# Kernel tuning notes

Hardware: AMD Instinct MI355X
Metric: run time of the kernel (lower is better)

## Reference

```python
import jax, jax.numpy as jnp
import numpy as np
from jax import lax

LAMBDA_REG = 0.01


def setup_inputs() -> dict:
    key = jax.random.key(0)
    k1, k2 = jax.random.split(key)
    features = jax.random.normal(k1, (8192, 512), dtype=jnp.float32)
    attention_scores = jax.random.uniform(k2, (8192,), dtype=jnp.float32)
    return {"features": features, "attention_scores": attention_scores, "k": 256}


def _kernel_matrix(features, attention_scores, lambda_reg=LAMBDA_REG):
    # L_ij = sqrt(q_i q_j) * <f_i, f_j>/(|f_i||f_j|) + lambda * I
    fn = features / jnp.linalg.norm(features, axis=1, keepdims=True)
    S = fn @ fn.T                                   # [N, N] cosine similarity
    q = attention_scores
    L = jnp.sqrt(q[:, None] * q[None, :]) * S
    N = features.shape[0]
    return L + lambda_reg * jnp.eye(N, dtype=features.dtype)


def _greedy_map(L, k):
    # Fast greedy DPP MAP (Chen et al. 2018): incremental Cholesky.
    # Marginal log-det gain of adding item i to selected set Y is log d_i,
    # where d_i = L_ii - ||c_i||^2 is the Schur complement. argmax over d_i
    # equals argmax over logdet(L_{Y+i}) since logdet(L_{Y+i}) = logdet(L_Y) + log d_i.
    N = L.shape[0]

    def step(carry, t):
        d, cis, mask = carry                         # d:[N], cis:[k,N], mask:[N]
        j = jnp.argmax(jnp.where(mask, d, -jnp.inf))  # first max (matches torch '>' tie-break)
        # e_n = (L[j,n] - sum_t cis[t,j]*cis[t,n]) / sqrt(d_j); unused rows of cis are zero
        e = (L[j] - cis[:, j] @ cis) / jnp.sqrt(d[j])  # [N]
        cis = cis.at[t].set(e)
        return (d - e * e, cis, mask.at[j].set(False)), j

    init = (jnp.diagonal(L), jnp.zeros((k, N), L.dtype), jnp.ones(N, dtype=bool))
    _, idx = lax.scan(step, init, jnp.arange(k))
    return idx                                        # [k] int selected indices


def reference(features, attention_scores, k):
    L = _kernel_matrix(features, attention_scores)
    return _greedy_map(L, k)
```

## Files before the change

### kernel.cpp

```cpp
#include <hip/hip_runtime.h>
#include <math.h>
#include <stdint.h>


#define N 8192
#define D 512
#define K 256
#define LAMBDA_REG 0.01f
#define NBLK 256
#define NTHR 256
#define ROWS 32
#define RS   560
#define CS   68
#define CTS  264
#define SSTR 8
#define SCOPE __HIP_MEMORY_SCOPE_AGENT

typedef unsigned long long u64;
typedef float f32x4 __attribute__((ext_vector_type(4)));

struct __align__(8) Pick { float v; int i; };

__device__ __forceinline__ bool better(float av, int ai, float bv, int bi) {
    return (av > bv) || (av == bv && ai < bi);
}

__device__ __forceinline__ u64 pack_slot(float v, int idx, int tag) {
    unsigned hi = ((unsigned)tag << 13) | (unsigned)idx;
    return ((u64)hi << 32) | (u64)__float_as_uint(v);
}

__device__ __forceinline__ void bypass_store_u64(u64* p, u64 v) {
    asm volatile("global_store_dwordx2 %0, %1, off sc0 sc1"
                 :: "v"(p), "v"(v) : "memory");
}

__device__ __forceinline__ void bypass_store_f32x4(const f32x4* p, f32x4 v) {
    asm volatile("global_store_dwordx4 %0, %1, off sc0 sc1"
                 :: "v"(p), "v"(v) : "memory");
}

__global__ __launch_bounds__(NTHR, 1) void dpp_kernel(
        const float* __restrict__ F, const float* __restrict__ q,
        float* __restrict__ FN, float* __restrict__ cisT,
        u64* __restrict__ slots, u64* __restrict__ mbox,
        int* __restrict__ out)
{
    const int tid = threadIdx.x;
    const int blk = blockIdx.x;
    const int r   = tid >> 3;
    const int c   = tid & 7;
    const int n   = blk * ROWS + r;

    __shared__ __align__(16) float lds_fn[ROWS * RS];
    __shared__ __align__(16) float lds_ct[ROWS * CTS];
    __shared__ __align__(16) float lds_gj[8 * CS];
    __shared__ __align__(16) float lds_cj[K];
    __shared__ Pick lds_wave[NTHR / 64];
    __shared__ Pick lds_final;

    const f32x4* F4  = reinterpret_cast<const f32x4*>(F);
    f32x4*       FN4 = reinterpret_cast<f32x4*>(FN);

    float dloc, qn;
    bool  masked = false;
    {
        const f32x4* src = F4 + (size_t)n * (D / 4) + c * 16;
        float* frow = &lds_fn[r * RS + c * CS];
        float ss = 0.f;
        #pragma unroll
        for (int i = 0; i < 16; ++i) {
            f32x4 v = src[i];
            *reinterpret_cast<f32x4*>(frow + 4 * i) = v;
            ss = fmaf(v.x, v.x, ss); ss = fmaf(v.y, v.y, ss);
            ss = fmaf(v.z, v.z, ss); ss = fmaf(v.w, v.w, ss);
        }
        ss += __shfl_xor(ss, 1); ss += __shfl_xor(ss, 2); ss += __shfl_xor(ss, 4);
        const float norm = sqrtf(ss);
        f32x4* dst = FN4 + (size_t)n * (D / 4) + c * 16;
        float ssn = 0.f;
        #pragma unroll
        for (int i = 0; i < 16; ++i) {
            f32x4 v = *reinterpret_cast<f32x4*>(frow + 4 * i);
            v.x /= norm; v.y /= norm; v.z /= norm; v.w /= norm;
            *reinterpret_cast<f32x4*>(frow + 4 * i) = v;
            bypass_store_f32x4(dst + i, v);
            ssn = fmaf(v.x, v.x, ssn); ssn = fmaf(v.y, v.y, ssn);
            ssn = fmaf(v.z, v.z, ssn); ssn = fmaf(v.w, v.w, ssn);
        }
        ssn += __shfl_xor(ssn, 1); ssn += __shfl_xor(ssn, 2); ssn += __shfl_xor(ssn, 4);
        qn = q[n];
        dloc = fmaf(sqrtf(qn * qn), ssn, LAMBDA_REG);
    }

    {
        float v = dloc; int idx = n;
        #pragma unroll
        for (int m = 32; m > 0; m >>= 1) {
            float ov = __shfl_xor(v, m);
            int   oi = __shfl_xor(idx, m);
            if (better(ov, oi, v, idx)) { v = ov; idx = oi; }
        }
        if ((tid & 63) == 0) { lds_wave[tid >> 6].v = v; lds_wave[tid >> 6].i = idx; }
        asm volatile("s_waitcnt vmcnt(0)" ::: "memory");
        __syncthreads();
        if (tid == 0) {
            Pick p = lds_wave[0];
            #pragma unroll
            for (int w = 1; w < NTHR / 64; ++w) {
                Pick o = lds_wave[w];
                if (better(o.v, o.i, p.v, p.i)) p = o;
            }
            bypass_store_u64(&slots[blk * SSTR], pack_slot(p.v, p.i, 0));
        }
    }

    for (int t = 0; t < K; ++t) {
        const unsigned want = (unsigned)t;

        if (blk == 0) {
            if (tid < 64) {
                const u64* pb = slots + (t & 1) * NBLK * SSTR;
                u64 x0, x1, x2, x3;
                while (true) {
                    x0 = __hip_atomic_load(pb + (tid * 4 + 0) * SSTR, __ATOMIC_RELAXED, SCOPE);
                    x1 = __hip_atomic_load(pb + (tid * 4 + 1) * SSTR, __ATOMIC_RELAXED, SCOPE);
                    x2 = __hip_atomic_load(pb + (tid * 4 + 2) * SSTR, __ATOMIC_RELAXED, SCOPE);
                    x3 = __hip_atomic_load(pb + (tid * 4 + 3) * SSTR, __ATOMIC_RELAXED, SCOPE);
                    bool ok = ((unsigned)(x0 >> 45) == want) &&
                              ((unsigned)(x1 >> 45) == want) &&
                              ((unsigned)(x2 >> 45) == want) &&
                              ((unsigned)(x3 >> 45) == want);
                    if (__all(ok)) break;
                    __builtin_amdgcn_s_sleep(1);
                }
                asm volatile("" ::: "memory");
                float v = __uint_as_float((unsigned)x0);
                int idx = (int)((x0 >> 32) & 8191u);
                {
                    float w = __uint_as_float((unsigned)x1); int k1 = (int)((x1 >> 32) & 8191u);
                    if (better(w, k1, v, idx)) { v = w; idx = k1; }
                    w = __uint_as_float((unsigned)x2); k1 = (int)((x2 >> 32) & 8191u);
                    if (better(w, k1, v, idx)) { v = w; idx = k1; }
                    w = __uint_as_float((unsigned)x3); k1 = (int)((x3 >> 32) & 8191u);
                    if (better(w, k1, v, idx)) { v = w; idx = k1; }
                }
                #pragma unroll
                for (int m = 32; m > 0; m >>= 1) {
                    float ov = __shfl_xor(v, m);
                    int   oi = __shfl_xor(idx, m);
                    if (better(ov, oi, v, idx)) { v = ov; idx = oi; }
                }
                const u64 msg = pack_slot(v, idx, t);
                u64* mb = mbox + (t & 1) * NBLK * SSTR;
                bypass_store_u64(mb + (tid * 4 + 0) * SSTR, msg);
                bypass_store_u64(mb + (tid * 4 + 1) * SSTR, msg);
                bypass_store_u64(mb + (tid * 4 + 2) * SSTR, msg);
                bypass_store_u64(mb + (tid * 4 + 3) * SSTR, msg);
                if (tid == 0) { lds_final.v = v; lds_final.i = idx; }
            }
        } else {
            if (tid == 0) {
                const u64* mp = mbox + ((t & 1) * NBLK + blk) * SSTR;
                u64 x;
                while (true) {
                    x = __hip_atomic_load(mp, __ATOMIC_RELAXED, SCOPE);
                    if ((unsigned)(x >> 45) == want) break;
                    __builtin_amdgcn_s_sleep(1);
                }
                asm volatile("" ::: "memory");
                lds_final.v = __uint_as_float((unsigned)x);
                lds_final.i = (int)((x >> 32) & 8191u);
            }
        }
        __syncthreads();
        const float dj = lds_final.v;
        const int   j  = lds_final.i;

        if (blk == 0 && tid == 0) out[t] = j;
        if (t == K - 1) break;

        const float sj = sqrtf(dj);
        const float qj = q[j];

        f32x4 gv;
        float cv;
        if (tid < 128) gv = FN4[(size_t)j * (D / 4) + tid];
        if (tid < t)   cv = cisT[(size_t)j * K + tid];
        if (tid < 128)
            *reinterpret_cast<f32x4*>(&lds_gj[(tid >> 4) * CS + (tid & 15) * 4]) = gv;
        if (tid < t)   lds_cj[tid] = cv;
        __syncthreads();

        const float* frow = &lds_fn[r * RS + c * CS];
        const float* grow = &lds_gj[c * CS];
        f32x4 a = {0.f, 0.f, 0.f, 0.f};
        #pragma unroll
        for (int i = 0; i < 16; ++i) {
            f32x4 v = *reinterpret_cast<const f32x4*>(frow + 4 * i);
            f32x4 g = *reinterpret_cast<const f32x4*>(grow + 4 * i);
            a.x = fmaf(v.x, g.x, a.x); a.y = fmaf(v.y, g.y, a.y);
            a.z = fmaf(v.z, g.z, a.z); a.w = fmaf(v.w, g.w, a.w);
        }
        float dot = (a.x + a.y) + (a.z + a.w);
        dot += __shfl_xor(dot, 1); dot += __shfl_xor(dot, 2); dot += __shfl_xor(dot, 4);
        float Ljn = sqrtf(qj * qn) * dot;
        if (n == j) Ljn += LAMBDA_REG;

        float cd = 0.f;
        const float* ctrow = &lds_ct[r * CTS];
        for (int tt = c; tt < t; tt += 8)
            cd = fmaf(lds_cj[tt], ctrow[tt], cd);
        cd += __shfl_xor(cd, 1); cd += __shfl_xor(cd, 2); cd += __shfl_xor(cd, 4);

        const float e = (Ljn - cd) / sj;
        if (c == 0) {
            lds_ct[r * CTS + t] = e;
            const float* ep = cisT + (size_t)n * K + t;
            asm volatile("global_store_dword %0, %1, off sc0 sc1"
                         :: "v"(ep), "v"(e) : "memory");
        }
        dloc = fmaf(-e, e, dloc);
        if (n == j) masked = true;

        {
            float v = masked ? -INFINITY : dloc; int idx = n;
            #pragma unroll
            for (int m = 32; m > 0; m >>= 1) {
                float ov = __shfl_xor(v, m);
                int   oi = __shfl_xor(idx, m);
                if (better(ov, oi, v, idx)) { v = ov; idx = oi; }
            }
            if ((tid & 63) == 0) { lds_wave[tid >> 6].v = v; lds_wave[tid >> 6].i = idx; }
        }
        asm volatile("s_waitcnt vmcnt(0)" ::: "memory");
        __syncthreads();
        if (tid == 0) {
            Pick p = lds_wave[0];
            #pragma unroll
            for (int w = 1; w < NTHR / 64; ++w) {
                Pick o = lds_wave[w];
                if (better(o.v, o.i, p.v, p.i)) p = o;
            }
            bypass_store_u64(&slots[(((t + 1) & 1) * NBLK + blk) * SSTR],
                             pack_slot(p.v, p.i, t + 1));
        }
    }
}

extern "C" void kernel_launch(void* const* d_in, const int* in_sizes, int n_in,
                              void* d_out, int out_size, void* d_ws, size_t ws_size,
                              hipStream_t stream) {
    const float* F = (const float*)d_in[0];
    const float* q = (const float*)d_in[1];
    int* out = (int*)d_out;

    uint8_t* w = (uint8_t*)d_ws;
    u64*   slots = (u64*)(w + 4096);
    u64*   mbox  = (u64*)(w + 4096 + 32768);
    float* FN    = (float*)(w + 131072);
    float* cisT  = (float*)(w + 131072 + (size_t)N * D * 4);

    hipMemsetAsync((void*)w, 0xFF, 131072, stream);
    hipLaunchKernelGGL(dpp_kernel, dim3(NBLK), dim3(NTHR), 0, stream,
                       F, q, FN, cisT, slots, mbox, out);
}
```

Before: 1.286 ms.

## Replace two-hop mailbox broadcast with redundant per-block argmax over all slots

```diff
diff --git a/kernel.cpp b/kernel.cpp
--- a/kernel.cpp
+++ b/kernel.cpp
@@ -43,8 +43,7 @@
 __global__ __launch_bounds__(NTHR, 1) void dpp_kernel(
         const float* __restrict__ F, const float* __restrict__ q,
         float* __restrict__ FN, float* __restrict__ cisT,
-        u64* __restrict__ slots, u64* __restrict__ mbox,
-        int* __restrict__ out)
+        u64* __restrict__ slots, int* __restrict__ out)
 {
     const int tid = threadIdx.x;
     const int blk = blockIdx.x;
@@ -118,60 +117,39 @@
     for (int t = 0; t < K; ++t) {
         const unsigned want = (unsigned)t;
 
-        if (blk == 0) {
-            if (tid < 64) {
-                const u64* pb = slots + (t & 1) * NBLK * SSTR;
-                u64 x0, x1, x2, x3;
-                while (true) {
-                    x0 = __hip_atomic_load(pb + (tid * 4 + 0) * SSTR, __ATOMIC_RELAXED, SCOPE);
-                    x1 = __hip_atomic_load(pb + (tid * 4 + 1) * SSTR, __ATOMIC_RELAXED, SCOPE);
-                    x2 = __hip_atomic_load(pb + (tid * 4 + 2) * SSTR, __ATOMIC_RELAXED, SCOPE);
-                    x3 = __hip_atomic_load(pb + (tid * 4 + 3) * SSTR, __ATOMIC_RELAXED, SCOPE);
-                    bool ok = ((unsigned)(x0 >> 45) == want) &&
-                              ((unsigned)(x1 >> 45) == want) &&
-                              ((unsigned)(x2 >> 45) == want) &&
-                              ((unsigned)(x3 >> 45) == want);
-                    if (__all(ok)) break;
-                    __builtin_amdgcn_s_sleep(1);
-                }
-                asm volatile("" ::: "memory");
-                float v = __uint_as_float((unsigned)x0);
-                int idx = (int)((x0 >> 32) & 8191u);
-                {
-                    float w = __uint_as_float((unsigned)x1); int k1 = (int)((x1 >> 32) & 8191u);
-                    if (better(w, k1, v, idx)) { v = w; idx = k1; }
-                    w = __uint_as_float((unsigned)x2); k1 = (int)((x2 >> 32) & 8191u);
-                    if (better(w, k1, v, idx)) { v = w; idx = k1; }
-                    w = __uint_as_float((unsigned)x3); k1 = (int)((x3 >> 32) & 8191u);
-                    if (better(w, k1, v, idx)) { v = w; idx = k1; }
-                }
-                #pragma unroll
-                for (int m = 32; m > 0; m >>= 1) {
-                    float ov = __shfl_xor(v, m);
-                    int   oi = __shfl_xor(idx, m);
-                    if (better(ov, oi, v, idx)) { v = ov; idx = oi; }
-                }
-                const u64 msg = pack_slot(v, idx, t);
-                u64* mb = mbox + (t & 1) * NBLK * SSTR;
-                bypass_store_u64(mb + (tid * 4 + 0) * SSTR, msg);
-                bypass_store_u64(mb + (tid * 4 + 1) * SSTR, msg);
-                bypass_store_u64(mb + (tid * 4 + 2) * SSTR, msg);
-                bypass_store_u64(mb + (tid * 4 + 3) * SSTR, msg);
-                if (tid == 0) { lds_final.v = v; lds_final.i = idx; }
-            }
-        } else {
-            if (tid == 0) {
-                const u64* mp = mbox + ((t & 1) * NBLK + blk) * SSTR;
-                u64 x;
-                while (true) {
-                    x = __hip_atomic_load(mp, __ATOMIC_RELAXED, SCOPE);
-                    if ((unsigned)(x >> 45) == want) break;
-                    __builtin_amdgcn_s_sleep(1);
-                }
-                asm volatile("" ::: "memory");
-                lds_final.v = __uint_as_float((unsigned)x);
-                lds_final.i = (int)((x >> 32) & 8191u);
-            }
+        if (tid < 64) {
+            const u64* pb = slots + (t & 1) * NBLK * SSTR;
+            u64 x0, x1, x2, x3;
+            while (true) {
+                x0 = __hip_atomic_load(pb + (tid * 4 + 0) * SSTR, __ATOMIC_RELAXED, SCOPE);
+                x1 = __hip_atomic_load(pb + (tid * 4 + 1) * SSTR, __ATOMIC_RELAXED, SCOPE);
+                x2 = __hip_atomic_load(pb + (tid * 4 + 2) * SSTR, __ATOMIC_RELAXED, SCOPE);
+                x3 = __hip_atomic_load(pb + (tid * 4 + 3) * SSTR, __ATOMIC_RELAXED, SCOPE);
+                bool ok = ((unsigned)(x0 >> 45) == want) &&
+                          ((unsigned)(x1 >> 45) == want) &&
+                          ((unsigned)(x2 >> 45) == want) &&
+                          ((unsigned)(x3 >> 45) == want);
+                if (__all(ok)) break;
+                __builtin_amdgcn_s_sleep(1);
+            }
+            asm volatile("" ::: "memory");
+            float v = __uint_as_float((unsigned)x0);
+            int idx = (int)((x0 >> 32) & 8191u);
+            {
+                float w = __uint_as_float((unsigned)x1); int k1 = (int)((x1 >> 32) & 8191u);
+                if (better(w, k1, v, idx)) { v = w; idx = k1; }
+                w = __uint_as_float((unsigned)x2); k1 = (int)((x2 >> 32) & 8191u);
+                if (better(w, k1, v, idx)) { v = w; idx = k1; }
+                w = __uint_as_float((unsigned)x3); k1 = (int)((x3 >> 32) & 8191u);
+                if (better(w, k1, v, idx)) { v = w; idx = k1; }
+            }
+            #pragma unroll
+            for (int m = 32; m > 0; m >>= 1) {
+                float ov = __shfl_xor(v, m);
+                int   oi = __shfl_xor(idx, m);
+                if (better(ov, oi, v, idx)) { v = ov; idx = oi; }
+            }
+            if (tid == 0) { lds_final.v = v; lds_final.i = idx; }
         }
         __syncthreads();
         const float dj = lds_final.v;
@@ -184,12 +162,20 @@
         const float qj = q[j];
 
         f32x4 gv;
-        float cv;
-        if (tid < 128) gv = FN4[(size_t)j * (D / 4) + tid];
-        if (tid < t)   cv = cisT[(size_t)j * K + tid];
-        if (tid < 128)
+        float cv0, cv1;
+        int   tt0 = tid - 128, tt1 = tid;
+        if (tid < 128) {
+            gv = FN4[(size_t)j * (D / 4) + tid];
+        } else {
+            if (tt0 < t) cv0 = cisT[(size_t)j * K + tt0];
+            if (tt1 < t) cv1 = cisT[(size_t)j * K + tt1];
+        }
+        if (tid < 128) {
             *reinterpret_cast<f32x4*>(&lds_gj[(tid >> 4) * CS + (tid & 15) * 4]) = gv;
-        if (tid < t)   lds_cj[tid] = cv;
+        } else {
+            if (tt0 < t) lds_cj[tt0] = cv0;
+            if (tt1 < t) lds_cj[tt1] = cv1;
+        }
         __syncthreads();
 
         const float* frow = &lds_fn[r * RS + c * CS];
@@ -257,11 +243,10 @@
 
     uint8_t* w = (uint8_t*)d_ws;
     u64*   slots = (u64*)(w + 4096);
-    u64*   mbox  = (u64*)(w + 4096 + 32768);
     float* FN    = (float*)(w + 131072);
     float* cisT  = (float*)(w + 131072 + (size_t)N * D * 4);
 
-    hipMemsetAsync((void*)w, 0xFF, 131072, stream);
+    hipMemsetAsync((void*)w, 0xFF, 65536, stream);
     hipLaunchKernelGGL(dpp_kernel, dim3(NBLK), dim3(NTHR), 0, stream,
-                       F, q, FN, cisT, slots, mbox, out);
-}
+                       F, q, FN, cisT, slots, out);
+}
```

Measured after the change: 1.177 ms. -8.5%, faster.
